# Performance work log

Hardware: AMD Instinct MI355X
Metric: run time of the kernel (lower is better)

The kernel has to match this reference:

```python
import jax, jax.numpy as jnp
import numpy as np

B, S, IN_F, OUT_F = 4, 2048, 4096, 4096

def setup_inputs() -> dict:
    key = jax.random.key(0)
    k1, k2, k3 = jax.random.split(key, 3)
    # int8 activations and weights (symmetric range)
    x = jax.random.randint(k1, (B, S, IN_F), -128, 128, dtype=jnp.int32).astype(jnp.int8)
    weight_q = jax.random.randint(k2, (OUT_F, IN_F), -128, 128, dtype=jnp.int32).astype(jnp.int8)
    scale_x = jnp.float32(0.05)   # activation quant scale
    scale_w = jnp.float32(0.02)   # weight quant scale (scalar, per-tensor)
    scale_y = jax.random.uniform(k3, (OUT_F,), minval=0.5, maxval=2.0, dtype=jnp.float32)  # per-output-row scale
    return {"x": x, "weight_q": weight_q, "scale_x": scale_x, "scale_w": scale_w, "scale_y": scale_y}

def reference(x, weight_q, scale_x, scale_w, scale_y):
    # int8 GEMM with int32 accumulation: [B,S,IN] @ [OUT,IN]^T -> [B,S,OUT]
    acc = jax.lax.dot_general(x, weight_q, ((((2,), (1,)), ((), ()))),
                              preferred_element_type=jnp.int32)
    # fused requantization scale: scale_x * scale_w / scale_y  -> [OUT]
    requant_scale = (scale_x * scale_w / scale_y).astype(jnp.float32)
    out_f = acc.astype(jnp.float32) * requant_scale  # broadcast over last dim
    out_q = jnp.clip(jnp.round(out_f), -128, 127).astype(jnp.int8)
    return out_q, scale_y
```

## Files before the change

kernel.cpp:

```cpp
#include <hip/hip_runtime.h>
#include <cstdint>


#define MDIM 8192
#define NDIM 4096
#define KDIM 4096
#define BM 128
#define BN 128
#define BK 64

typedef int v4i __attribute__((ext_vector_type(4)));

__device__ __forceinline__ uint32_t pack4(int a, int b, int c, int d) {
  return (uint32_t)(a & 0xFF) | ((uint32_t)(b & 0xFF) << 8) |
         ((uint32_t)(c & 0xFF) << 16) | ((uint32_t)(d & 0xFF) << 24);
}

__global__ __launch_bounds__(256) void pack_kernel(
    const int* __restrict__ x32, const int* __restrict__ w32,
    const float* __restrict__ sy, uint8_t* __restrict__ x8,
    uint8_t* __restrict__ w8, float* __restrict__ tail) {
  size_t idx = (size_t)blockIdx.x * blockDim.x + threadIdx.x;
  if (idx < (size_t)NDIM) tail[idx] = sy[idx];
  const size_t NX = (size_t)MDIM * KDIM;
  const size_t NW = (size_t)NDIM * KDIM;
  size_t base = idx * 16;
  const int* src;
  uint8_t* dst;
  if (base < NX) {
    src = x32 + base;
    dst = x8 + base;
  } else if (base < NX + NW) {
    src = w32 + (base - NX);
    dst = w8 + (base - NX);
  } else {
    return;
  }
  v4i a0 = *(const v4i*)(src + 0);
  v4i a1 = *(const v4i*)(src + 4);
  v4i a2 = *(const v4i*)(src + 8);
  v4i a3 = *(const v4i*)(src + 12);
  v4i o;
  o[0] = (int)pack4(a0[0], a0[1], a0[2], a0[3]);
  o[1] = (int)pack4(a1[0], a1[1], a1[2], a1[3]);
  o[2] = (int)pack4(a2[0], a2[1], a2[2], a2[3]);
  o[3] = (int)pack4(a3[0], a3[1], a3[2], a3[3]);
  *(v4i*)dst = o;
}

__global__ __launch_bounds__(256) void tail_kernel(const float* __restrict__ sy,
                                                   float* __restrict__ tail) {
  int i = blockIdx.x * blockDim.x + threadIdx.x;
  if (i < NDIM) tail[i] = sy[i];
}

template <int PACKED>
__global__ __launch_bounds__(256) void gemm_kernel(
    const uint8_t* __restrict__ A8, const uint8_t* __restrict__ B8,
    const int* __restrict__ A32, const int* __restrict__ B32,
    const float* __restrict__ sxp, const float* __restrict__ swp,
    const float* __restrict__ syp, float* __restrict__ out) {
  __shared__ __align__(16) uint8_t As[BM][BK];
  __shared__ __align__(16) uint8_t Bs[BN][BK];

  const int tid = threadIdx.x;
  const int lane = tid & 63;
  const int wave = tid >> 6;

  const int nwg = (MDIM / BM) * (NDIM / BN);
  const int cpx = nwg / 8;
  int orig = blockIdx.x;
  int wg = (orig % 8) * cpx + orig / 8;
  const int ntn = NDIM / BN;
  int tm = wg / ntn, tn = wg % ntn;
  const int rowBase = tm * BM, colBase = tn * BN;

  const int wm = (wave >> 1) * 64;
  const int wn = (wave & 1) * 64;

  const int srow = wave * 16 + (lane >> 2);
  const int scol = (lane & 3) * 16;

  const int kl = lane >> 4;
  const int fr = lane & 15;

  v4i acc[4][4];
#pragma unroll
  for (int i = 0; i < 4; i++)
#pragma unroll
    for (int j = 0; j < 4; j++) acc[i][j] = (v4i){0, 0, 0, 0};

  for (int kt = 0; kt < KDIM; kt += BK) {
    if (PACKED) {
      const uint8_t* ag = A8 + (size_t)(rowBase + srow) * KDIM + kt + scol;
      const uint8_t* bg = B8 + (size_t)(colBase + srow) * KDIM + kt + scol;
      __builtin_amdgcn_global_load_lds(
          (const __attribute__((address_space(1))) void*)ag,
          (__attribute__((address_space(3))) void*)(&As[srow][scol]), 16, 0, 0);
      __builtin_amdgcn_global_load_lds(
          (const __attribute__((address_space(1))) void*)(ag + (size_t)64 * KDIM),
          (__attribute__((address_space(3))) void*)(&As[64 + srow][scol]), 16, 0, 0);
      __builtin_amdgcn_global_load_lds(
          (const __attribute__((address_space(1))) void*)bg,
          (__attribute__((address_space(3))) void*)(&Bs[srow][scol]), 16, 0, 0);
      __builtin_amdgcn_global_load_lds(
          (const __attribute__((address_space(1))) void*)(bg + (size_t)64 * KDIM),
          (__attribute__((address_space(3))) void*)(&Bs[64 + srow][scol]), 16, 0, 0);
    } else {
#pragma unroll
      for (int c = 0; c < 2; ++c) {
        const int* ag = A32 + (size_t)(rowBase + c * 64 + srow) * KDIM + kt + scol;
        v4i p0 = *(const v4i*)(ag + 0), p1 = *(const v4i*)(ag + 4);
        v4i p2 = *(const v4i*)(ag + 8), p3 = *(const v4i*)(ag + 12);
        v4i oa;
        oa[0] = (int)pack4(p0[0], p0[1], p0[2], p0[3]);
        oa[1] = (int)pack4(p1[0], p1[1], p1[2], p1[3]);
        oa[2] = (int)pack4(p2[0], p2[1], p2[2], p2[3]);
        oa[3] = (int)pack4(p3[0], p3[1], p3[2], p3[3]);
        *(v4i*)&As[c * 64 + srow][scol] = oa;
        const int* bgp = B32 + (size_t)(colBase + c * 64 + srow) * KDIM + kt + scol;
        v4i q0 = *(const v4i*)(bgp + 0), q1 = *(const v4i*)(bgp + 4);
        v4i q2 = *(const v4i*)(bgp + 8), q3 = *(const v4i*)(bgp + 12);
        v4i ob;
        ob[0] = (int)pack4(q0[0], q0[1], q0[2], q0[3]);
        ob[1] = (int)pack4(q1[0], q1[1], q1[2], q1[3]);
        ob[2] = (int)pack4(q2[0], q2[1], q2[2], q2[3]);
        ob[3] = (int)pack4(q3[0], q3[1], q3[2], q3[3]);
        *(v4i*)&Bs[c * 64 + srow][scol] = ob;
      }
    }
    __syncthreads();

    v4i af[4], bf[4];
#pragma unroll
    for (int i = 0; i < 4; i++)
      af[i] = *(const v4i*)&As[wm + i * 16 + fr][kl * 16];
#pragma unroll
    for (int j = 0; j < 4; j++)
      bf[j] = *(const v4i*)&Bs[wn + j * 16 + fr][kl * 16];
#pragma unroll
    for (int i = 0; i < 4; i++)
#pragma unroll
      for (int j = 0; j < 4; j++)
        acc[i][j] =
            __builtin_amdgcn_mfma_i32_16x16x64_i8(af[i], bf[j], acc[i][j], 0, 0, 0);
    __syncthreads();
  }

  const float s = sxp[0] * swp[0];
#pragma unroll
  for (int j = 0; j < 4; j++) {
    const int col = colBase + wn + j * 16 + fr;
    const float rs = s / syp[col];
#pragma unroll
    for (int i = 0; i < 4; i++) {
      const int row0 = rowBase + wm + i * 16 + kl * 4;
#pragma unroll
      for (int r = 0; r < 4; r++) {
        float v = rintf((float)acc[i][j][r] * rs);
        v = fminf(127.f, fmaxf(-128.f, v));
        out[(size_t)(row0 + r) * NDIM + col] = v;
      }
    }
  }
}

extern "C" void kernel_launch(void* const* d_in, const int* in_sizes, int n_in,
                              void* d_out, int out_size, void* d_ws, size_t ws_size,
                              hipStream_t stream) {
  const int* x32 = (const int*)d_in[0];
  const int* w32 = (const int*)d_in[1];
  const float* sx = (const float*)d_in[2];
  const float* sw = (const float*)d_in[3];
  const float* sy = (const float*)d_in[4];
  float* out = (float*)d_out;
  float* tail = out + (size_t)MDIM * NDIM;

  const size_t need = (size_t)MDIM * KDIM + (size_t)NDIM * KDIM;
  const int nblocks_gemm = (MDIM / BM) * (NDIM / BN);

  if (ws_size >= need) {
    uint8_t* x8 = (uint8_t*)d_ws;
    uint8_t* w8 = x8 + (size_t)MDIM * KDIM;
    const int total16 = (int)(need / 16);
    pack_kernel<<<(total16 + 255) / 256, 256, 0, stream>>>(x32, w32, sy, x8, w8,
                                                           tail);
    gemm_kernel<1><<<nblocks_gemm, 256, 0, stream>>>(x8, w8, nullptr, nullptr, sx,
                                                     sw, sy, out);
  } else {
    tail_kernel<<<(NDIM + 255) / 256, 256, 0, stream>>>(sy, tail);
    gemm_kernel<0><<<nblocks_gemm, 256, 0, stream>>>(nullptr, nullptr, x32, w32,
                                                     sx, sw, sy, out);
  }
}
```

Baseline: 225.3 us.

## Use 256x256 tiles with a 4-stage LDS ring, prefetch and swizzled layout

The GEMM moves to 256x256 tiles with 512 threads, each wave computing 128x64. Global-to-LDS loads now run two k-steps ahead through a 4-slot ring buffer, so each iteration needs one barrier and loads overlap with the MFMA work. An XOR swizzle on the 16-byte chunks is meant to avoid LDS bank conflicts on fragment reads. The unpacked fallback path is removed, so the code now always relies on the workspace being large enough, and the 128KB LDS per block limits occupancy.

New measurement: 195.0 us. -13.5%, faster.

```diff
diff --git a/kernel.cpp b/kernel.cpp
--- a/kernel.cpp
+++ b/kernel.cpp
@@ -5,11 +5,20 @@
 #define MDIM 8192
 #define NDIM 4096
 #define KDIM 4096
-#define BM 128
-#define BN 128
-#define BK 64
+#define BM 256
+#define BN 256
+#define BKB 64
+#define NT (KDIM / BKB)
 
 typedef int v4i __attribute__((ext_vector_type(4)));
+
+#define FENCE() asm volatile("" ::: "memory")
+#define BAR()                         \
+  do {                                \
+    FENCE();                          \
+    __builtin_amdgcn_s_barrier();     \
+    FENCE();                          \
+  } while (0)
 
 __device__ __forceinline__ uint32_t pack4(int a, int b, int c, int d) {
   return (uint32_t)(a & 0xFF) | ((uint32_t)(b & 0xFF) << 8) |
@@ -48,20 +57,11 @@
   *(v4i*)dst = o;
 }
 
-__global__ __launch_bounds__(256) void tail_kernel(const float* __restrict__ sy,
-                                                   float* __restrict__ tail) {
-  int i = blockIdx.x * blockDim.x + threadIdx.x;
-  if (i < NDIM) tail[i] = sy[i];
-}
-
-template <int PACKED>
-__global__ __launch_bounds__(256) void gemm_kernel(
+__global__ __launch_bounds__(512, 2) void gemm_kernel(
     const uint8_t* __restrict__ A8, const uint8_t* __restrict__ B8,
-    const int* __restrict__ A32, const int* __restrict__ B32,
     const float* __restrict__ sxp, const float* __restrict__ swp,
     const float* __restrict__ syp, float* __restrict__ out) {
-  __shared__ __align__(16) uint8_t As[BM][BK];
-  __shared__ __align__(16) uint8_t Bs[BN][BK];
+  __shared__ __align__(16) uint8_t lds[131072];
 
   const int tid = threadIdx.x;
   const int lane = tid & 63;
@@ -69,92 +69,92 @@
 
   const int nwg = (MDIM / BM) * (NDIM / BN);
   const int cpx = nwg / 8;
-  int orig = blockIdx.x;
-  int wg = (orig % 8) * cpx + orig / 8;
+  const int wg = ((int)blockIdx.x % 8) * cpx + (int)blockIdx.x / 8;
   const int ntn = NDIM / BN;
-  int tm = wg / ntn, tn = wg % ntn;
-  const int rowBase = tm * BM, colBase = tn * BN;
+  const int rowBase = (wg / ntn) * BM;
+  const int colBase = (wg % ntn) * BN;
 
-  const int wm = (wave >> 1) * 64;
-  const int wn = (wave & 1) * 64;
+  const int wm2 = wave >> 2;
+  const int wn4 = wave & 3;
 
   const int srow = wave * 16 + (lane >> 2);
-  const int scol = (lane & 3) * 16;
+  const int scol = (((lane & 3) ^ ((lane >> 2) & 3)) << 4);
+  const uint32_t sdst = (uint32_t)(wave * 1024 + lane * 16);
 
   const int kl = lane >> 4;
   const int fr = lane & 15;
+  const int swz = ((kl ^ (fr & 3)) << 4);
 
-  v4i acc[4][4];
+  uint32_t a_off[8], b_off[4];
 #pragma unroll
-  for (int i = 0; i < 4; i++)
+  for (int i = 0; i < 8; i++)
+    a_off[i] = (uint32_t)((wm2 * 128 + i * 16 + fr) * 64 + swz);
+#pragma unroll
+  for (int j = 0; j < 4; j++)
+    b_off[j] = (uint32_t)(65536 + (wn4 * 64 + j * 16 + fr) * 64 + swz);
+
+  v4i acc[8][4];
+#pragma unroll
+  for (int i = 0; i < 8; i++)
 #pragma unroll
     for (int j = 0; j < 4; j++) acc[i][j] = (v4i){0, 0, 0, 0};
 
-  for (int kt = 0; kt < KDIM; kt += BK) {
-    if (PACKED) {
-      const uint8_t* ag = A8 + (size_t)(rowBase + srow) * KDIM + kt + scol;
-      const uint8_t* bg = B8 + (size_t)(colBase + srow) * KDIM + kt + scol;
-      __builtin_amdgcn_global_load_lds(
-          (const __attribute__((address_space(1))) void*)ag,
-          (__attribute__((address_space(3))) void*)(&As[srow][scol]), 16, 0, 0);
-      __builtin_amdgcn_global_load_lds(
-          (const __attribute__((address_space(1))) void*)(ag + (size_t)64 * KDIM),
-          (__attribute__((address_space(3))) void*)(&As[64 + srow][scol]), 16, 0, 0);
-      __builtin_amdgcn_global_load_lds(
-          (const __attribute__((address_space(1))) void*)bg,
-          (__attribute__((address_space(3))) void*)(&Bs[srow][scol]), 16, 0, 0);
-      __builtin_amdgcn_global_load_lds(
-          (const __attribute__((address_space(1))) void*)(bg + (size_t)64 * KDIM),
-          (__attribute__((address_space(3))) void*)(&Bs[64 + srow][scol]), 16, 0, 0);
-    } else {
+  auto stage = [&](int t) {
+    const uint32_t ab = (uint32_t)(t & 3) * 16384u;
+    const uint8_t* ga = A8 + (size_t)(rowBase + srow) * KDIM + t * BKB + scol;
+    const uint8_t* gb = B8 + (size_t)(colBase + srow) * KDIM + t * BKB + scol;
+    __builtin_amdgcn_global_load_lds(
+        (const __attribute__((address_space(1))) void*)ga,
+        (__attribute__((address_space(3))) void*)(lds + ab + sdst), 16, 0, 0);
+    __builtin_amdgcn_global_load_lds(
+        (const __attribute__((address_space(1))) void*)(ga + (size_t)128 * KDIM),
+        (__attribute__((address_space(3))) void*)(lds + ab + 8192 + sdst), 16, 0, 0);
+    __builtin_amdgcn_global_load_lds(
+        (const __attribute__((address_space(1))) void*)gb,
+        (__attribute__((address_space(3))) void*)(lds + 65536 + ab + sdst), 16, 0,
+        0);
+    __builtin_amdgcn_global_load_lds(
+        (const __attribute__((address_space(1))) void*)(gb + (size_t)128 * KDIM),
+        (__attribute__((address_space(3))) void*)(lds + 65536 + ab + 8192 + sdst),
+        16, 0, 0);
+  };
+
+  stage(0);
+  stage(1);
+
+  for (int t = 0; t < NT; ++t) {
+    if (t < NT - 1)
+      asm volatile("s_waitcnt vmcnt(4)" ::: "memory");
+    else
+      asm volatile("s_waitcnt vmcnt(0)" ::: "memory");
+    BAR();
+
+    if (t + 2 < NT) stage(t + 2);
+
+    const uint8_t* Ab = lds + (uint32_t)(t & 3) * 16384u;
+    v4i af[8], bf[4];
 #pragma unroll
-      for (int c = 0; c < 2; ++c) {
-        const int* ag = A32 + (size_t)(rowBase + c * 64 + srow) * KDIM + kt + scol;
-        v4i p0 = *(const v4i*)(ag + 0), p1 = *(const v4i*)(ag + 4);
-        v4i p2 = *(const v4i*)(ag + 8), p3 = *(const v4i*)(ag + 12);
-        v4i oa;
-        oa[0] = (int)pack4(p0[0], p0[1], p0[2], p0[3]);
-        oa[1] = (int)pack4(p1[0], p1[1], p1[2], p1[3]);
-        oa[2] = (int)pack4(p2[0], p2[1], p2[2], p2[3]);
-        oa[3] = (int)pack4(p3[0], p3[1], p3[2], p3[3]);
-        *(v4i*)&As[c * 64 + srow][scol] = oa;
-        const int* bgp = B32 + (size_t)(colBase + c * 64 + srow) * KDIM + kt + scol;
-        v4i q0 = *(const v4i*)(bgp + 0), q1 = *(const v4i*)(bgp + 4);
-        v4i q2 = *(const v4i*)(bgp + 8), q3 = *(const v4i*)(bgp + 12);
-        v4i ob;
-        ob[0] = (int)pack4(q0[0], q0[1], q0[2], q0[3]);
-        ob[1] = (int)pack4(q1[0], q1[1], q1[2], q1[3]);
-        ob[2] = (int)pack4(q2[0], q2[1], q2[2], q2[3]);
-        ob[3] = (int)pack4(q3[0], q3[1], q3[2], q3[3]);
-        *(v4i*)&Bs[c * 64 + srow][scol] = ob;
-      }
-    }
-    __syncthreads();
-
-    v4i af[4], bf[4];
+    for (int i = 0; i < 8; i++) af[i] = *(const v4i*)(Ab + a_off[i]);
 #pragma unroll
-    for (int i = 0; i < 4; i++)
-      af[i] = *(const v4i*)&As[wm + i * 16 + fr][kl * 16];
+    for (int j = 0; j < 4; j++) bf[j] = *(const v4i*)(Ab + b_off[j]);
 #pragma unroll
-    for (int j = 0; j < 4; j++)
-      bf[j] = *(const v4i*)&Bs[wn + j * 16 + fr][kl * 16];
-#pragma unroll
-    for (int i = 0; i < 4; i++)
+    for (int i = 0; i < 8; i++)
 #pragma unroll
       for (int j = 0; j < 4; j++)
         acc[i][j] =
             __builtin_amdgcn_mfma_i32_16x16x64_i8(af[i], bf[j], acc[i][j], 0, 0, 0);
-    __syncthreads();
   }
 
   const float s = sxp[0] * swp[0];
+  const int wrow = rowBase + wm2 * 128;
+  const int wcol = colBase + wn4 * 64;
 #pragma unroll
   for (int j = 0; j < 4; j++) {
-    const int col = colBase + wn + j * 16 + fr;
+    const int col = wcol + j * 16 + fr;
     const float rs = s / syp[col];
 #pragma unroll
-    for (int i = 0; i < 4; i++) {
-      const int row0 = rowBase + wm + i * 16 + kl * 4;
+    for (int i = 0; i < 8; i++) {
+      const int row0 = wrow + i * 16 + kl * 4;
 #pragma unroll
       for (int r = 0; r < 4; r++) {
         float v = rintf((float)acc[i][j][r] * rs);
@@ -176,20 +176,15 @@
   float* out = (float*)d_out;
   float* tail = out + (size_t)MDIM * NDIM;
 
+  uint8_t* x8 = (uint8_t*)d_ws;
+  uint8_t* w8 = x8 + (size_t)MDIM * KDIM;
   const size_t need = (size_t)MDIM * KDIM + (size_t)NDIM * KDIM;
-  const int nblocks_gemm = (MDIM / BM) * (NDIM / BN);
+  (void)need;
 
-  if (ws_size >= need) {
-    uint8_t* x8 = (uint8_t*)d_ws;
-    uint8_t* w8 = x8 + (size_t)MDIM * KDIM;
-    const int total16 = (int)(need / 16);
-    pack_kernel<<<(total16 + 255) / 256, 256, 0, stream>>>(x32, w32, sy, x8, w8,
-                                                           tail);
-    gemm_kernel<1><<<nblocks_gemm, 256, 0, stream>>>(x8, w8, nullptr, nullptr, sx,
-                                                     sw, sy, out);
-  } else {
-    tail_kernel<<<(NDIM + 255) / 256, 256, 0, stream>>>(sy, tail);
-    gemm_kernel<0><<<nblocks_gemm, 256, 0, stream>>>(nullptr, nullptr, x32, w32,
-                                                     sx, sw, sy, out);
-  }
+  const int total16 = (int)(((size_t)MDIM * KDIM + (size_t)NDIM * KDIM) / 16);
+  pack_kernel<<<(total16 + 255) / 256, 256, 0, stream>>>(x32, w32, sy, x8, w8,
+                                                         tail);
+
+  const int nblocks = (MDIM / BM) * (NDIM / BN);
+  gemm_kernel<<<nblocks, 512, 0, stream>>>(x8, w8, sx, sw, sy, out);
 }
```
